# Performance work log

Measured on AMD Instinct MI355X. Metric: run time of the kernel, lower is better.

The kernel has to match this reference:

```python
import jax, jax.numpy as jnp
import numpy as np

NUM_GROUPS = 32
NUM_HEADS = 8
EPS = 1e-5
RESCALE = 1.0


def _group_norm(x, gamma, beta):
    # x: [B, C, H, W]
    B, C, H, W = x.shape
    xg = x.reshape(B, NUM_GROUPS, C // NUM_GROUPS, H, W)
    mu = xg.mean(axis=(2, 3, 4), keepdims=True)
    var = jnp.mean(jnp.square(xg - mu), axis=(2, 3, 4), keepdims=True)
    xn = ((xg - mu) * jax.lax.rsqrt(var + EPS)).reshape(B, C, H, W)
    return xn * gamma[None, :, None, None] + beta[None, :, None, None]


def _layer_norm(x, gamma, beta):
    mu = x.mean(axis=-1, keepdims=True)
    var = jnp.mean(jnp.square(x - mu), axis=-1, keepdims=True)
    return (x - mu) * jax.lax.rsqrt(var + EPS) * gamma + beta


def setup_inputs() -> dict:
    key = jax.random.key(0)
    ks = jax.random.split(key, 12)
    C = 512
    B, H, W = 8, 32, 32
    s = 1.0 / np.sqrt(C)
    return {
        "hidden_states": jax.random.normal(ks[0], (B, C, H, W), jnp.float32),
        "gn_gamma": jnp.ones((C,), jnp.float32),
        "gn_beta": jnp.zeros((C,), jnp.float32),
        "wq": jax.random.normal(ks[1], (C, C), jnp.float32) * s,
        "bq": jnp.zeros((C,), jnp.float32),
        "wk": jax.random.normal(ks[2], (C, C), jnp.float32) * s,
        "bk": jnp.zeros((C,), jnp.float32),
        "wv": jax.random.normal(ks[3], (C, C), jnp.float32) * s,
        "bv": jnp.zeros((C,), jnp.float32),
        "wo": jax.random.normal(ks[4], (C, C), jnp.float32) * s,
        "bo": jnp.zeros((C,), jnp.float32),
        "ln_gamma": jnp.ones((C,), jnp.float32),
        "ln_beta": jnp.zeros((C,), jnp.float32),
    }


def reference(hidden_states, gn_gamma, gn_beta, wq, bq, wk, bk, wv, bv, wo, bo, ln_gamma, ln_beta):
    residual = hidden_states
    B, C, H, W = hidden_states.shape
    x = _group_norm(hidden_states, gn_gamma, gn_beta)
    x = x.reshape(B, C, H * W).transpose(0, 2, 1)  # [B, T, C]
    q = x @ wq.T + bq
    k = x @ wk.T + bk
    v = x @ wv.T + bv
    T = H * W
    dh = C // NUM_HEADS
    q = q.reshape(B, T, NUM_HEADS, dh).transpose(0, 2, 1, 3)  # [B, h, T, d]
    k = k.reshape(B, T, NUM_HEADS, dh).transpose(0, 2, 1, 3)
    v = v.reshape(B, T, NUM_HEADS, dh).transpose(0, 2, 1, 3)
    scale = 1.0 / np.sqrt(np.sqrt(dh))  # applied to q only, as in the source
    scores = jnp.einsum('bhid,bhjd->bhij', q * scale, k)
    probs = jax.nn.softmax(scores.astype(jnp.float32), axis=-1).astype(scores.dtype)
    ctx = jnp.einsum('bhij,bhjd->bhid', probs, v)  # [B, h, T, d]
    ctx = ctx.transpose(0, 2, 1, 3).reshape(B, T, C)
    out = _layer_norm(ctx @ wo.T + bo, ln_gamma, ln_beta)
    out = out.transpose(0, 2, 1).reshape(B, C, H, W)
    return (out + residual) / RESCALE
```

## Files before the change

### kernel.cpp

```cpp
#include <hip/hip_runtime.h>
#include <math.h>
#include <stdint.h>

#define BB 8
#define CC 512
#define TT 1024
#define NG 32
#define CPG 16
static constexpr float EPS = 1e-5f;
static constexpr float QSCALE = 0.35355339059327373f;

typedef __attribute__((ext_vector_type(4))) float f32x4;
typedef __attribute__((ext_vector_type(8))) short s16x8;

__device__ __forceinline__ unsigned short bf16_hi(float x) {
    union { float f; unsigned u; } c; c.f = x;
    unsigned r = c.u + 0x7FFFu + ((c.u >> 16) & 1u);
    return (unsigned short)(r >> 16);
}
__device__ __forceinline__ float bf16_f(unsigned short h) {
    union { unsigned u; float f; } c; c.u = ((unsigned)h) << 16;
    return c.f;
}
__device__ __forceinline__ void split2(float x, unsigned short& h, unsigned short& l) {
    h = bf16_hi(x);
    l = bf16_hi(x - bf16_f(h));
}

__device__ __forceinline__ f32x4 mfma3(s16x8 ah, s16x8 al, s16x8 bh, s16x8 bl, f32x4 c) {
    c = __builtin_amdgcn_mfma_f32_16x16x32_bf16(ah, bh, c, 0, 0, 0);
    c = __builtin_amdgcn_mfma_f32_16x16x32_bf16(ah, bl, c, 0, 0, 0);
    c = __builtin_amdgcn_mfma_f32_16x16x32_bf16(al, bh, c, 0, 0, 0);
    return c;
}

__device__ __forceinline__ int kswz(int row, int ch) { return ch ^ (row & 7); }
__device__ __forceinline__ int pswz(int row, int ch) { return ch ^ (((row >> 2) & 3) << 1); }

__global__ __launch_bounds__(256) void gn_stats_kernel(const float* __restrict__ x,
                                                       float* __restrict__ stats) {
    int bg = blockIdx.x;
    const float* base = x + (size_t)bg * (CPG * TT);
    float s = 0.f, ss = 0.f;
    for (int f = threadIdx.x; f < (CPG * TT) / 4; f += 256) {
        float4 v = *(const float4*)(base + 4 * f);
        s  += v.x + v.y + v.z + v.w;
        ss += v.x * v.x + v.y * v.y + v.z * v.z + v.w * v.w;
    }
    for (int off = 32; off; off >>= 1) {
        s  += __shfl_down(s, off);
        ss += __shfl_down(ss, off);
    }
    __shared__ float rs[4], rss[4];
    int wid = threadIdx.x >> 6, lane = threadIdx.x & 63;
    if (lane == 0) { rs[wid] = s; rss[wid] = ss; }
    __syncthreads();
    if (threadIdx.x == 0) {
        float S = rs[0] + rs[1] + rs[2] + rs[3];
        float SS = rss[0] + rss[1] + rss[2] + rss[3];
        const float invN = 1.f / (CPG * TT);
        float mu = S * invN;
        float var = SS * invN - mu * mu;
        stats[bg * 2]     = mu;
        stats[bg * 2 + 1] = rsqrtf(var + EPS);
    }
}

__global__ __launch_bounds__(256) void gn_apply_kernel(const float* __restrict__ x,
                                                       const float* __restrict__ stats,
                                                       const float* __restrict__ gamma,
                                                       const float* __restrict__ beta,
                                                       unsigned short* __restrict__ xh,
                                                       unsigned short* __restrict__ xl) {
    __shared__ float tile[32][33];
    int c0 = blockIdx.x << 5, t0 = blockIdx.y << 5, b = blockIdx.z;
    int tx = threadIdx.x, ty = threadIdx.y;
#pragma unroll
    for (int k = 0; k < 32; k += 8) {
        int c = c0 + ty + k;
        float mu   = stats[(b * NG + (c >> 4)) * 2];
        float rstd = stats[(b * NG + (c >> 4)) * 2 + 1];
        float v = x[((size_t)(b * CC + c)) * TT + t0 + tx];
        tile[ty + k][tx] = (v - mu) * rstd * gamma[c] + beta[c];
    }
    __syncthreads();
#pragma unroll
    for (int k = 0; k < 32; k += 8) {
        int t = t0 + ty + k;
        float v = tile[tx][ty + k];
        size_t idx = ((size_t)(b * TT + t)) * CC + c0 + tx;
        unsigned short h, l; split2(v, h, l);
        xh[idx] = h; xl[idx] = l;
    }
}

__global__ __launch_bounds__(256) void wsplit_kernel(const float* __restrict__ wq,
                                                     const float* __restrict__ wk,
                                                     const float* __restrict__ wv,
                                                     const float* __restrict__ wo,
                                                     unsigned short* __restrict__ wh,
                                                     unsigned short* __restrict__ wl) {
    int wid = blockIdx.y;
    const float* src = (wid == 0) ? wq : (wid == 1) ? wk : (wid == 2) ? wv : wo;
    int base = (blockIdx.x * 256 + threadIdx.x) * 8;
    float4 a = *(const float4*)(src + base);
    float4 b = *(const float4*)(src + base + 4);
    float v[8] = {a.x, a.y, a.z, a.w, b.x, b.y, b.z, b.w};
    s16x8 h, l;
#pragma unroll
    for (int i = 0; i < 8; ++i) {
        unsigned short hh, ll; split2(v[i], hh, ll);
        h[i] = (short)hh; l[i] = (short)ll;
    }
    *(s16x8*)(wh + (size_t)wid * 262144 + base) = h;
    *(s16x8*)(wl + (size_t)wid * 262144 + base) = l;
}

__device__ __forceinline__ void gemm_main(const unsigned short* __restrict__ ah,
                                          const unsigned short* __restrict__ al,
                                          const unsigned short* __restrict__ wh,
                                          const unsigned short* __restrict__ wl,
                                          int i0, int j0, f32x4 (&acc)[4][4]) {
    __shared__ unsigned short As[128 * 64], Bs[128 * 64];
    int tid = threadIdx.x;
    int lane = tid & 63, wv = tid >> 6;
    int lr = lane & 15, lg = lane >> 4;
    int wr = wv >> 1, wc = wv & 1;
    const f32x4 z4 = {0.f, 0.f, 0.f, 0.f};
#pragma unroll
    for (int m = 0; m < 4; ++m)
#pragma unroll
        for (int n = 0; n < 4; ++n) acc[m][n] = z4;

    for (int k0 = 0; k0 < 512; k0 += 32) {
        __syncthreads();
#pragma unroll
        for (int u = 0; u < 4; ++u) {
            int f = u * 256 + tid;
            int row = f >> 3, s = f & 7;
            int pl = s >> 2, ck = s & 3;
            const unsigned short* asrc = (pl ? al : ah) + (size_t)(i0 + row) * 512 + k0 + ck * 8;
            const unsigned short* bsrc = (pl ? wl : wh) + (size_t)(j0 + row) * 512 + k0 + ck * 8;
            int d = row * 64 + (kswz(row, s) << 3);
            *(s16x8*)&As[d] = *(const s16x8*)asrc;
            *(s16x8*)&Bs[d] = *(const s16x8*)bsrc;
        }
        __syncthreads();

        s16x8 aH[4], aL[4], bH[4], bL[4];
#pragma unroll
        for (int m = 0; m < 4; ++m) {
            int row = wr * 64 + m * 16 + lr;
            aH[m] = *(const s16x8*)&As[row * 64 + (kswz(row, lg) << 3)];
            aL[m] = *(const s16x8*)&As[row * 64 + (kswz(row, lg + 4) << 3)];
        }
#pragma unroll
        for (int n = 0; n < 4; ++n) {
            int row = wc * 64 + n * 16 + lr;
            bH[n] = *(const s16x8*)&Bs[row * 64 + (kswz(row, lg) << 3)];
            bL[n] = *(const s16x8*)&Bs[row * 64 + (kswz(row, lg + 4) << 3)];
        }
#pragma unroll
        for (int m = 0; m < 4; ++m)
#pragma unroll
            for (int n = 0; n < 4; ++n)
                acc[m][n] = mfma3(aH[m], aL[m], bH[n], bL[n], acc[m][n]);
    }
}

__global__ __launch_bounds__(256) void qkv_gemm_kernel(
        const unsigned short* __restrict__ xh, const unsigned short* __restrict__ xl,
        const unsigned short* __restrict__ whA, const unsigned short* __restrict__ wlA,
        const float* __restrict__ bq, const float* __restrict__ bk, const float* __restrict__ bv,
        unsigned short* qh, unsigned short* ql, unsigned short* kh, unsigned short* kl,
        unsigned short* vh, unsigned short* vl) {
    int z = blockIdx.z;
    const unsigned short* wh = whA + (size_t)z * 262144;
    const unsigned short* wl = wlA + (size_t)z * 262144;
    const float* bias = (z == 0) ? bq : (z == 1) ? bk : bv;
    unsigned short* dh = (z == 0) ? qh : (z == 1) ? kh : vh;
    unsigned short* dl = (z == 0) ? ql : (z == 1) ? kl : vl;
    float scale = (z == 0) ? QSCALE : 1.f;
    int j0 = blockIdx.x << 7, i0 = blockIdx.y << 7;
    f32x4 acc[4][4];
    gemm_main(xh, xl, wh, wl, i0, j0, acc);
    int tid = threadIdx.x, lane = tid & 63, wv = tid >> 6;
    int lr = lane & 15, lg = lane >> 4, wr = wv >> 1, wc = wv & 1;
#pragma unroll
    for (int n = 0; n < 4; ++n) {
        int j = j0 + wc * 64 + n * 16 + lr;
        float bj = bias[j];
#pragma unroll
        for (int m = 0; m < 4; ++m)
#pragma unroll
            for (int r = 0; r < 4; ++r) {
                int i = i0 + wr * 64 + m * 16 + lg * 4 + r;
                float v = (acc[m][n][r] + bj) * scale;
                size_t off = (((size_t)(i >> 10) * 8 + (j >> 6)) << 16)
                             + (size_t)(i & 1023) * 64 + (j & 63);
                unsigned short hh, ll; split2(v, hh, ll);
                dh[off] = hh; dl[off] = ll;
            }
    }
}

__global__ __launch_bounds__(256) void proj_gemm_kernel(
        const unsigned short* __restrict__ ch, const unsigned short* __restrict__ cl,
        const unsigned short* __restrict__ wh, const unsigned short* __restrict__ wl,
        const float* __restrict__ bo, float* __restrict__ Y) {
    int j0 = blockIdx.x << 7, i0 = blockIdx.y << 7;
    f32x4 acc[4][4];
    gemm_main(ch, cl, wh, wl, i0, j0, acc);
    int tid = threadIdx.x, lane = tid & 63, wv = tid >> 6;
    int lr = lane & 15, lg = lane >> 4, wr = wv >> 1, wc = wv & 1;
#pragma unroll
    for (int n = 0; n < 4; ++n) {
        int j = j0 + wc * 64 + n * 16 + lr;
        float bj = bo[j];
#pragma unroll
        for (int m = 0; m < 4; ++m)
#pragma unroll
            for (int r = 0; r < 4; ++r) {
                int i = i0 + wr * 64 + m * 16 + lg * 4 + r;
                Y[(size_t)i * 512 + j] = acc[m][n][r] + bj;
            }
    }
}

__global__ __launch_bounds__(256) void attn_mfma_kernel(
        const unsigned short* __restrict__ qh, const unsigned short* __restrict__ ql,
        const unsigned short* __restrict__ kh, const unsigned short* __restrict__ kl,
        const unsigned short* __restrict__ vh, const unsigned short* __restrict__ vl,
        unsigned short* __restrict__ ch, unsigned short* __restrict__ cl) {
    __shared__ unsigned short Qh[64 * 64], Ql[64 * 64], Kh_[64 * 64], Kl_[64 * 64],
                              Vth[64 * 64], Vtl[64 * 64], Ph[64 * 64], Pl[64 * 64];
    int id = blockIdx.x;
    int fid = (id & 7) * 128 + (id >> 3);
    int bh = fid >> 4, qt = fid & 15;
    int tid = threadIdx.x, lane = tid & 63, w = tid >> 6;
    int lr = lane & 15, lg = lane >> 4;
    size_t pbase = (size_t)bh << 16;

#pragma unroll
    for (int u = 0; u < 2; ++u) {
        int f = u * 256 + tid;
        int row = f >> 3, s = f & 7;
        int d = row * 64 + (kswz(row, s) << 3);
        size_t g = pbase + (size_t)(qt * 64 + row) * 64 + s * 8;
        *(s16x8*)&Qh[d] = *(const s16x8*)(qh + g);
        *(s16x8*)&Ql[d] = *(const s16x8*)(ql + g);
    }
    float m_[4], l_[4];
    f32x4 o[4];
    const f32x4 z4 = {0.f, 0.f, 0.f, 0.f};
#pragma unroll
    for (int r = 0; r < 4; ++r) { m_[r] = -INFINITY; l_[r] = 0.f; }
#pragma unroll
    for (int n = 0; n < 4; ++n) o[n] = z4;

    for (int kt = 0; kt < 16; ++kt) {
        __syncthreads();
#pragma unroll
        for (int u = 0; u < 2; ++u) {
            int f = u * 256 + tid;
            int row = f >> 3, s = f & 7;
            int d = row * 64 + (kswz(row, s) << 3);
            size_t g = pbase + (size_t)(kt * 64 + row) * 64 + s * 8;
            *(s16x8*)&Kh_[d] = *(const s16x8*)(kh + g);
            *(s16x8*)&Kl_[d] = *(const s16x8*)(kl + g);
        }
        {
            int t = lane, dg = w;
            size_t g = pbase + (size_t)(kt * 64 + t) * 64 + dg * 16;
            s16x8 h0 = *(const s16x8*)(vh + g), h1 = *(const s16x8*)(vh + g + 8);
            s16x8 l0 = *(const s16x8*)(vl + g), l1 = *(const s16x8*)(vl + g + 8);
#pragma unroll
            for (int i = 0; i < 8; ++i) {
                int d0 = dg * 16 + i, d1 = dg * 16 + 8 + i;
                int o0 = d0 * 64 + (kswz(d0, t >> 3) << 3) + (t & 7);
                int o1 = d1 * 64 + (kswz(d1, t >> 3) << 3) + (t & 7);
                Vth[o0] = (unsigned short)h0[i]; Vth[o1] = (unsigned short)h1[i];
                Vtl[o0] = (unsigned short)l0[i]; Vtl[o1] = (unsigned short)l1[i];
            }
        }
        __syncthreads();

        f32x4 s4[4];
#pragma unroll
        for (int n = 0; n < 4; ++n) s4[n] = z4;
#pragma unroll
        for (int c = 0; c < 2; ++c) {
            int arow = w * 16 + lr;
            s16x8 aH = *(const s16x8*)&Qh[arow * 64 + (kswz(arow, lg + 4 * c) << 3)];
            s16x8 aL = *(const s16x8*)&Ql[arow * 64 + (kswz(arow, lg + 4 * c) << 3)];
#pragma unroll
            for (int n = 0; n < 4; ++n) {
                int brow = n * 16 + lr;
                s16x8 bH = *(const s16x8*)&Kh_[brow * 64 + (kswz(brow, lg + 4 * c) << 3)];
                s16x8 bL = *(const s16x8*)&Kl_[brow * 64 + (kswz(brow, lg + 4 * c) << 3)];
                s4[n] = mfma3(aH, aL, bH, bL, s4[n]);
            }
        }

        float p[4][4];
#pragma unroll
        for (int r = 0; r < 4; ++r) {
            float rmax = fmaxf(fmaxf(s4[0][r], s4[1][r]), fmaxf(s4[2][r], s4[3][r]));
            rmax = fmaxf(rmax, __shfl_xor(rmax, 1));
            rmax = fmaxf(rmax, __shfl_xor(rmax, 2));
            rmax = fmaxf(rmax, __shfl_xor(rmax, 4));
            rmax = fmaxf(rmax, __shfl_xor(rmax, 8));
            float mnew = fmaxf(m_[r], rmax);
            float corr = __expf(m_[r] - mnew);
            float rsum = 0.f;
#pragma unroll
            for (int n = 0; n < 4; ++n) { p[n][r] = __expf(s4[n][r] - mnew); rsum += p[n][r]; }
            rsum += __shfl_xor(rsum, 1); rsum += __shfl_xor(rsum, 2);
            rsum += __shfl_xor(rsum, 4); rsum += __shfl_xor(rsum, 8);
            l_[r] = l_[r] * corr + rsum;
            m_[r] = mnew;
#pragma unroll
            for (int n = 0; n < 4; ++n) o[n][r] *= corr;
        }

#pragma unroll
        for (int n = 0; n < 4; ++n)
#pragma unroll
            for (int r = 0; r < 4; ++r) {
                int prow = w * 16 + lg * 4 + r;
                int col = n * 16 + lr;
                int idx = prow * 64 + (pswz(prow, col >> 3) << 3) + (col & 7);
                unsigned short hh, ll; split2(p[n][r], hh, ll);
                Ph[idx] = hh; Pl[idx] = ll;
            }

#pragma unroll
        for (int c = 0; c < 2; ++c) {
            int prow = w * 16 + lr;
            int pidx = prow * 64 + (pswz(prow, lg + 4 * c) << 3);
            s16x8 aH = *(const s16x8*)&Ph[pidx];
            s16x8 aL = *(const s16x8*)&Pl[pidx];
#pragma unroll
            for (int n = 0; n < 4; ++n) {
                int vrow = n * 16 + lr;
                int vidx = vrow * 64 + (kswz(vrow, lg + 4 * c) << 3);
                s16x8 bH = *(const s16x8*)&Vth[vidx];
                s16x8 bL = *(const s16x8*)&Vtl[vidx];
                o[n] = mfma3(aH, aL, bH, bL, o[n]);
            }
        }
    }

    int b = bh >> 3, h = bh & 7;
#pragma unroll
    for (int r = 0; r < 4; ++r) {
        float inv = 1.f / l_[r];
        int t = qt * 64 + w * 16 + lg * 4 + r;
#pragma unroll
        for (int n = 0; n < 4; ++n) {
            int d = n * 16 + lr;
            float v = o[n][r] * inv;
            size_t off = ((size_t)(b * TT + t)) * 512 + h * 64 + d;
            unsigned short hh, ll; split2(v, hh, ll);
            ch[off] = hh; cl[off] = ll;
        }
    }
}

__global__ __launch_bounds__(256) void ln_res_kernel(const float* __restrict__ Y,
                                                     const float* __restrict__ resid,
                                                     const float* __restrict__ g,
                                                     const float* __restrict__ be,
                                                     float* __restrict__ out) {
    __shared__ float rows[32][516];
    __shared__ float mu_s[32], rs_s[32];
    int t0 = blockIdx.x << 5, b = blockIdx.y;
    int tid = threadIdx.x;
#pragma unroll
    for (int it = 0; it < 16; ++it) {
        int f = it * 256 + tid;
        int r = f >> 7, chn = f & 127;
        *(float4*)&rows[r][chn << 2] =
            *(const float4*)(Y + ((size_t)(b * TT) + t0 + r) * 512 + (chn << 2));
    }
    __syncthreads();
    {
        int r = tid >> 3, sub = tid & 7;
        float s = 0.f, ss = 0.f;
        for (int i = 0; i < 64; ++i) {
            float v = rows[r][sub + (i << 3)];
            s += v; ss += v * v;
        }
#pragma unroll
        for (int off = 1; off < 8; off <<= 1) { s += __shfl_xor(s, off); ss += __shfl_xor(ss, off); }
        if (sub == 0) {
            float mu = s * (1.f / 512.f);
            float var = ss * (1.f / 512.f) - mu * mu;
            mu_s[r] = mu; rs_s[r] = rsqrtf(var + EPS);
        }
    }
    __syncthreads();
    int j = tid & 31, crow = tid >> 5;
    for (int it = 0; it < 64; ++it) {
        int c = it * 8 + crow;
        float v = (rows[j][c] - mu_s[j]) * rs_s[j] * g[c] + be[c];
        size_t oidx = ((size_t)(b * 512) + c) * 1024 + t0 + j;
        out[oidx] = v + resid[oidx];
    }
}

extern "C" void kernel_launch(void* const* d_in, const int* in_sizes, int n_in,
                              void* d_out, int out_size, void* d_ws, size_t ws_size,
                              hipStream_t stream) {
    const float* x        = (const float*)d_in[0];
    const float* gn_gamma = (const float*)d_in[1];
    const float* gn_beta  = (const float*)d_in[2];
    const float* wq = (const float*)d_in[3];
    const float* bq = (const float*)d_in[4];
    const float* wk = (const float*)d_in[5];
    const float* bk = (const float*)d_in[6];
    const float* wv = (const float*)d_in[7];
    const float* bv = (const float*)d_in[8];
    const float* wo = (const float*)d_in[9];
    const float* bo = (const float*)d_in[10];
    const float* ln_gamma = (const float*)d_in[11];
    const float* ln_beta  = (const float*)d_in[12];
    float* out = (float*)d_out;

    char* W = (char*)d_ws;
    unsigned short* Xh  = (unsigned short*)(W);
    unsigned short* Xl  = (unsigned short*)(W + (8ull  << 20));
    unsigned short* WhA = (unsigned short*)(W + (16ull << 20));
    unsigned short* WlA = (unsigned short*)(W + (18ull << 20));
    unsigned short* Qh  = (unsigned short*)(W + (20ull << 20));
    unsigned short* Ql  = (unsigned short*)(W + (28ull << 20));
    unsigned short* Kh  = (unsigned short*)(W + (36ull << 20));
    unsigned short* Kl  = (unsigned short*)(W + (44ull << 20));
    float*          Y   = (float*)         (W + (20ull << 20));
    float*        stats = (float*)         (W + (52ull << 20));
    unsigned short* ctxh = Xh;
    unsigned short* ctxl = Xl;
    unsigned short* Vh  = (unsigned short*)d_out;
    unsigned short* Vl  = (unsigned short*)d_out + 4194304;

    gn_stats_kernel<<<dim3(BB * NG), dim3(256), 0, stream>>>(x, stats);
    gn_apply_kernel<<<dim3(CC / 32, TT / 32, BB), dim3(32, 8), 0, stream>>>(
        x, stats, gn_gamma, gn_beta, Xh, Xl);
    wsplit_kernel<<<dim3(128, 4), dim3(256), 0, stream>>>(wq, wk, wv, wo, WhA, WlA);
    qkv_gemm_kernel<<<dim3(4, 64, 3), dim3(256), 0, stream>>>(
        Xh, Xl, WhA, WlA, bq, bk, bv, Qh, Ql, Kh, Kl, Vh, Vl);
    attn_mfma_kernel<<<dim3(1024), dim3(256), 0, stream>>>(
        Qh, Ql, Kh, Kl, Vh, Vl, ctxh, ctxl);
    proj_gemm_kernel<<<dim3(4, 64), dim3(256), 0, stream>>>(
        ctxh, ctxl, WhA + 3ull * 262144, WlA + 3ull * 262144, bo, Y);
    ln_res_kernel<<<dim3(TT / 32, BB), dim3(256), 0, stream>>>(
        Y, x, ln_gamma, ln_beta, out);
}
```

Before: 314.5 us.

## Use direct global-to-LDS loads, pre-transpose V in QKV epilogue, keep Q in registers

The GEMM and attention tile loads now use the global_load_lds builtin, which writes global memory straight into shared memory without passing through VGPRs. The swizzle is encoded through per-lane source addresses so that each wave's destination stays contiguous. The QKV GEMM epilogue writes V already transposed (d-major), so the attention kernel no longer does a scalar LDS transpose of V on every tile. Q fragments are held in registers instead of LDS, which frees shared memory, at the cost of relying on the builtin's LDS address semantics being correct.

After: 309.6 us. Within noise of the previous version (-1.5%).

```diff
diff --git a/kernel.cpp b/kernel.cpp
--- a/kernel.cpp
+++ b/kernel.cpp
@@ -12,6 +12,7 @@
 
 typedef __attribute__((ext_vector_type(4))) float f32x4;
 typedef __attribute__((ext_vector_type(8))) short s16x8;
+typedef __attribute__((ext_vector_type(4))) short s16x4;
 
 __device__ __forceinline__ unsigned short bf16_hi(float x) {
     union { float f; unsigned u; } c; c.f = x;
@@ -32,6 +33,12 @@
     c = __builtin_amdgcn_mfma_f32_16x16x32_bf16(ah, bl, c, 0, 0, 0);
     c = __builtin_amdgcn_mfma_f32_16x16x32_bf16(al, bh, c, 0, 0, 0);
     return c;
+}
+
+__device__ __forceinline__ void gload16(const void* g, void* l) {
+    __builtin_amdgcn_global_load_lds((const __attribute__((address_space(1))) void*)g,
+                                     (__attribute__((address_space(3))) void*)l,
+                                     16, 0, 0);
 }
 
 __device__ __forceinline__ int kswz(int row, int ch) { return ch ^ (row & 7); }
@@ -132,18 +139,30 @@
 #pragma unroll
         for (int n = 0; n < 4; ++n) acc[m][n] = z4;
 
+    int l8 = lane >> 3, c8 = lane & 7;
+    int s = c8 ^ l8;
+    int pl = s >> 2, ck = s & 3;
+    const unsigned short* abase = pl ? al : ah;
+    const unsigned short* bbase = pl ? wl : wh;
+    const unsigned short* ap[4];
+    const unsigned short* bp[4];
+    unsigned short* ad[4];
+    unsigned short* bd[4];
+#pragma unroll
+    for (int u = 0; u < 4; ++u) {
+        int row = u * 32 + wv * 8 + l8;
+        ap[u] = abase + (size_t)(i0 + row) * 512 + ck * 8;
+        bp[u] = bbase + (size_t)(j0 + row) * 512 + ck * 8;
+        ad[u] = &As[u * 2048 + wv * 512];
+        bd[u] = &Bs[u * 2048 + wv * 512];
+    }
+
     for (int k0 = 0; k0 < 512; k0 += 32) {
         __syncthreads();
 #pragma unroll
         for (int u = 0; u < 4; ++u) {
-            int f = u * 256 + tid;
-            int row = f >> 3, s = f & 7;
-            int pl = s >> 2, ck = s & 3;
-            const unsigned short* asrc = (pl ? al : ah) + (size_t)(i0 + row) * 512 + k0 + ck * 8;
-            const unsigned short* bsrc = (pl ? wl : wh) + (size_t)(j0 + row) * 512 + k0 + ck * 8;
-            int d = row * 64 + (kswz(row, s) << 3);
-            *(s16x8*)&As[d] = *(const s16x8*)asrc;
-            *(s16x8*)&Bs[d] = *(const s16x8*)bsrc;
+            gload16(ap[u] + k0, ad[u]);
+            gload16(bp[u] + k0, bd[u]);
         }
         __syncthreads();
 
@@ -173,34 +192,58 @@
         const unsigned short* __restrict__ whA, const unsigned short* __restrict__ wlA,
         const float* __restrict__ bq, const float* __restrict__ bk, const float* __restrict__ bv,
         unsigned short* qh, unsigned short* ql, unsigned short* kh, unsigned short* kl,
-        unsigned short* vh, unsigned short* vl) {
+        unsigned short* vth, unsigned short* vtl) {
     int z = blockIdx.z;
     const unsigned short* wh = whA + (size_t)z * 262144;
     const unsigned short* wl = wlA + (size_t)z * 262144;
     const float* bias = (z == 0) ? bq : (z == 1) ? bk : bv;
-    unsigned short* dh = (z == 0) ? qh : (z == 1) ? kh : vh;
-    unsigned short* dl = (z == 0) ? ql : (z == 1) ? kl : vl;
-    float scale = (z == 0) ? QSCALE : 1.f;
     int j0 = blockIdx.x << 7, i0 = blockIdx.y << 7;
     f32x4 acc[4][4];
     gemm_main(xh, xl, wh, wl, i0, j0, acc);
     int tid = threadIdx.x, lane = tid & 63, wv = tid >> 6;
     int lr = lane & 15, lg = lane >> 4, wr = wv >> 1, wc = wv & 1;
-#pragma unroll
-    for (int n = 0; n < 4; ++n) {
-        int j = j0 + wc * 64 + n * 16 + lr;
-        float bj = bias[j];
-#pragma unroll
-        for (int m = 0; m < 4; ++m)
-#pragma unroll
-            for (int r = 0; r < 4; ++r) {
-                int i = i0 + wr * 64 + m * 16 + lg * 4 + r;
-                float v = (acc[m][n][r] + bj) * scale;
-                size_t off = (((size_t)(i >> 10) * 8 + (j >> 6)) << 16)
-                             + (size_t)(i & 1023) * 64 + (j & 63);
-                unsigned short hh, ll; split2(v, hh, ll);
-                dh[off] = hh; dl[off] = ll;
+    if (z == 2) {
+#pragma unroll
+        for (int n = 0; n < 4; ++n) {
+            int j = j0 + wc * 64 + n * 16 + lr;
+            int d = j & 63, h = j >> 6;
+            float bj = bias[j];
+#pragma unroll
+            for (int m = 0; m < 4; ++m) {
+                int ibase = i0 + wr * 64 + m * 16 + lg * 4;
+                s16x4 v4h, v4l;
+#pragma unroll
+                for (int r = 0; r < 4; ++r) {
+                    float v = acc[m][n][r] + bj;
+                    unsigned short hh, ll; split2(v, hh, ll);
+                    v4h[r] = (short)hh; v4l[r] = (short)ll;
+                }
+                size_t off = (((size_t)((ibase >> 10) * 8 + h)) << 16)
+                             + (size_t)d * 1024 + (ibase & 1023);
+                *(s16x4*)(vth + off) = v4h;
+                *(s16x4*)(vtl + off) = v4l;
             }
+        }
+    } else {
+        unsigned short* dh = (z == 0) ? qh : kh;
+        unsigned short* dl = (z == 0) ? ql : kl;
+        float scale = (z == 0) ? QSCALE : 1.f;
+#pragma unroll
+        for (int n = 0; n < 4; ++n) {
+            int j = j0 + wc * 64 + n * 16 + lr;
+            float bj = bias[j];
+#pragma unroll
+            for (int m = 0; m < 4; ++m)
+#pragma unroll
+                for (int r = 0; r < 4; ++r) {
+                    int i = i0 + wr * 64 + m * 16 + lg * 4 + r;
+                    float v = (acc[m][n][r] + bj) * scale;
+                    size_t off = (((size_t)(i >> 10) * 8 + (j >> 6)) << 16)
+                                 + (size_t)(i & 1023) * 64 + (j & 63);
+                    unsigned short hh, ll; split2(v, hh, ll);
+                    dh[off] = hh; dl[off] = ll;
+                }
+        }
     }
 }
 
@@ -230,26 +273,29 @@
 __global__ __launch_bounds__(256) void attn_mfma_kernel(
         const unsigned short* __restrict__ qh, const unsigned short* __restrict__ ql,
         const unsigned short* __restrict__ kh, const unsigned short* __restrict__ kl,
-        const unsigned short* __restrict__ vh, const unsigned short* __restrict__ vl,
+        const unsigned short* __restrict__ vth, const unsigned short* __restrict__ vtl,
         unsigned short* __restrict__ ch, unsigned short* __restrict__ cl) {
-    __shared__ unsigned short Qh[64 * 64], Ql[64 * 64], Kh_[64 * 64], Kl_[64 * 64],
-                              Vth[64 * 64], Vtl[64 * 64], Ph[64 * 64], Pl[64 * 64];
+    __shared__ unsigned short Kh[64 * 64], Kl[64 * 64],
+                              Vh[64 * 64], Vl[64 * 64],
+                              Ph[64 * 64], Pl[64 * 64];
     int id = blockIdx.x;
     int fid = (id & 7) * 128 + (id >> 3);
     int bh = fid >> 4, qt = fid & 15;
     int tid = threadIdx.x, lane = tid & 63, w = tid >> 6;
     int lr = lane & 15, lg = lane >> 4;
-    size_t pbase = (size_t)bh << 16;
-
-#pragma unroll
-    for (int u = 0; u < 2; ++u) {
-        int f = u * 256 + tid;
-        int row = f >> 3, s = f & 7;
-        int d = row * 64 + (kswz(row, s) << 3);
-        size_t g = pbase + (size_t)(qt * 64 + row) * 64 + s * 8;
-        *(s16x8*)&Qh[d] = *(const s16x8*)(qh + g);
-        *(s16x8*)&Ql[d] = *(const s16x8*)(ql + g);
-    }
+    const size_t pb = (size_t)bh << 16;
+
+    const unsigned short* qrow = qh + pb + (size_t)(qt * 64 + w * 16 + lr) * 64 + lg * 8;
+    const unsigned short* qrol = ql + pb + (size_t)(qt * 64 + w * 16 + lr) * 64 + lg * 8;
+    s16x8 qH0 = *(const s16x8*)(qrow);
+    s16x8 qH1 = *(const s16x8*)(qrow + 32);
+    s16x8 qL0 = *(const s16x8*)(qrol);
+    s16x8 qL1 = *(const s16x8*)(qrol + 32);
+
+    int l8 = lane >> 3, c8 = lane & 7;
+    int sch = c8 ^ l8;
+    int srow = w * 8 + l8;
+
     float m_[4], l_[4];
     f32x4 o[4];
     const f32x4 z4 = {0.f, 0.f, 0.f, 0.f};
@@ -261,27 +307,15 @@
     for (int kt = 0; kt < 16; ++kt) {
         __syncthreads();
 #pragma unroll
-        for (int u = 0; u < 2; ++u) {
-            int f = u * 256 + tid;
-            int row = f >> 3, s = f & 7;
-            int d = row * 64 + (kswz(row, s) << 3);
-            size_t g = pbase + (size_t)(kt * 64 + row) * 64 + s * 8;
-            *(s16x8*)&Kh_[d] = *(const s16x8*)(kh + g);
-            *(s16x8*)&Kl_[d] = *(const s16x8*)(kl + g);
-        }
-        {
-            int t = lane, dg = w;
-            size_t g = pbase + (size_t)(kt * 64 + t) * 64 + dg * 16;
-            s16x8 h0 = *(const s16x8*)(vh + g), h1 = *(const s16x8*)(vh + g + 8);
-            s16x8 l0 = *(const s16x8*)(vl + g), l1 = *(const s16x8*)(vl + g + 8);
-#pragma unroll
-            for (int i = 0; i < 8; ++i) {
-                int d0 = dg * 16 + i, d1 = dg * 16 + 8 + i;
-                int o0 = d0 * 64 + (kswz(d0, t >> 3) << 3) + (t & 7);
-                int o1 = d1 * 64 + (kswz(d1, t >> 3) << 3) + (t & 7);
-                Vth[o0] = (unsigned short)h0[i]; Vth[o1] = (unsigned short)h1[i];
-                Vtl[o0] = (unsigned short)l0[i]; Vtl[o1] = (unsigned short)l1[i];
-            }
+        for (int v = 0; v < 2; ++v) {
+            int row = v * 32 + srow;
+            size_t kg = pb + (size_t)(kt * 64 + row) * 64 + sch * 8;
+            size_t vg = pb + (size_t)row * 1024 + kt * 64 + sch * 8;
+            int db = v * 2048 + w * 512;
+            gload16(kh + kg, &Kh[db]);
+            gload16(kl + kg, &Kl[db]);
+            gload16(vth + vg, &Vh[db]);
+            gload16(vtl + vg, &Vl[db]);
         }
         __syncthreads();
 
@@ -290,15 +324,13 @@
         for (int n = 0; n < 4; ++n) s4[n] = z4;
 #pragma unroll
         for (int c = 0; c < 2; ++c) {
-            int arow = w * 16 + lr;
-            s16x8 aH = *(const s16x8*)&Qh[arow * 64 + (kswz(arow, lg + 4 * c) << 3)];
-            s16x8 aL = *(const s16x8*)&Ql[arow * 64 + (kswz(arow, lg + 4 * c) << 3)];
+            s16x8 aH = c ? qH1 : qH0;
+            s16x8 aL = c ? qL1 : qL0;
 #pragma unroll
             for (int n = 0; n < 4; ++n) {
                 int brow = n * 16 + lr;
-                s16x8 bH = *(const s16x8*)&Kh_[brow * 64 + (kswz(brow, lg + 4 * c) << 3)];
-                s16x8 bL = *(const s16x8*)&Kl_[brow * 64 + (kswz(brow, lg + 4 * c) << 3)];
-                s4[n] = mfma3(aH, aL, bH, bL, s4[n]);
+                int pos = brow * 64 + (((c * 4 + lg) ^ (brow & 7)) << 3);
+                s4[n] = mfma3(aH, aL, *(const s16x8*)&Kh[pos], *(const s16x8*)&Kl[pos], s4[n]);
             }
         }
 
@@ -337,16 +369,14 @@
 #pragma unroll
         for (int c = 0; c < 2; ++c) {
             int prow = w * 16 + lr;
-            int pidx = prow * 64 + (pswz(prow, lg + 4 * c) << 3);
+            int pidx = prow * 64 + (pswz(prow, c * 4 + lg) << 3);
             s16x8 aH = *(const s16x8*)&Ph[pidx];
             s16x8 aL = *(const s16x8*)&Pl[pidx];
 #pragma unroll
             for (int n = 0; n < 4; ++n) {
                 int vrow = n * 16 + lr;
-                int vidx = vrow * 64 + (kswz(vrow, lg + 4 * c) << 3);
-                s16x8 bH = *(const s16x8*)&Vth[vidx];
-                s16x8 bL = *(const s16x8*)&Vtl[vidx];
-                o[n] = mfma3(aH, aL, bH, bL, o[n]);
+                int vidx = vrow * 64 + (((c * 4 + lg) ^ (vrow & 7)) << 3);
+                o[n] = mfma3(aH, aL, *(const s16x8*)&Vh[vidx], *(const s16x8*)&Vl[vidx], o[n]);
             }
         }
     }
@@ -440,17 +470,17 @@
     float*        stats = (float*)         (W + (52ull << 20));
     unsigned short* ctxh = Xh;
     unsigned short* ctxl = Xl;
-    unsigned short* Vh  = (unsigned short*)d_out;
-    unsigned short* Vl  = (unsigned short*)d_out + 4194304;
+    unsigned short* Vth = (unsigned short*)d_out;
+    unsigned short* Vtl = (unsigned short*)d_out + 4194304;
 
     gn_stats_kernel<<<dim3(BB * NG), dim3(256), 0, stream>>>(x, stats);
     gn_apply_kernel<<<dim3(CC / 32, TT / 32, BB), dim3(32, 8), 0, stream>>>(
         x, stats, gn_gamma, gn_beta, Xh, Xl);
     wsplit_kernel<<<dim3(128, 4), dim3(256), 0, stream>>>(wq, wk, wv, wo, WhA, WlA);
     qkv_gemm_kernel<<<dim3(4, 64, 3), dim3(256), 0, stream>>>(
-        Xh, Xl, WhA, WlA, bq, bk, bv, Qh, Ql, Kh, Kl, Vh, Vl);
+        Xh, Xl, WhA, WlA, bq, bk, bv, Qh, Ql, Kh, Kl, Vth, Vtl);
     attn_mfma_kernel<<<dim3(1024), dim3(256), 0, stream>>>(
-        Qh, Ql, Kh, Kl, Vh, Vl, ctxh, ctxl);
+        Qh, Ql, Kh, Kl, Vth, Vtl, ctxh, ctxl);
     proj_gemm_kernel<<<dim3(4, 64), dim3(256), 0, stream>>>(
         ctxh, ctxl, WhA + 3ull * 262144, WlA + 3ull * 262144, bo, Y);
     ln_res_kernel<<<dim3(TT / 32, BB), dim3(256), 0, stream>>>(
```
